# Performance work log

Measured on AMD Instinct MI355X. Metric: run time of the kernel, lower is better.

## Reference

```python
import jax, jax.numpy as jnp
import numpy as np
import math

B, L, DIM = 2, 2048, 1024
NUM_HEADS, QUANTUM_HEADS, CHUNK = 16, 2, 64
HD = DIM // NUM_HEADS  # 64 == CHUNK (required by the original broadcast)
TH = NUM_HEADS - QUANTUM_HEADS
STEPS = 2048
LN_EPS = 1e-5


def setup_inputs() -> dict:
    key = jax.random.key(0)
    ks = jax.random.split(key, 12)
    inp = {
        'x': jax.random.normal(ks[0], (B, L, DIM), dtype=jnp.float32),
        # to_quantum_state: Linear(HD, 2HD) + LayerNorm(2HD) + Tanh
        'wq1': jax.random.normal(ks[1], (HD, 2 * HD), dtype=jnp.float32) * 0.05,
        'bq1': jnp.zeros((2 * HD,), dtype=jnp.float32),
        'ln_g': jnp.ones((2 * HD,), dtype=jnp.float32),
        'ln_b': jnp.zeros((2 * HD,), dtype=jnp.float32),
        'phase_shifts': jax.random.normal(ks[2], (QUANTUM_HEADS,), dtype=jnp.float32) * 0.02,
        'freqs': jax.random.normal(ks[3], (QUANTUM_HEADS,), dtype=jnp.float32) * 0.02,
        # traditional heads: q/k/v projections, no bias
        'wq': jax.random.normal(ks[4], (DIM, TH * HD), dtype=jnp.float32) * 0.02,
        'wk': jax.random.normal(ks[5], (DIM, TH * HD), dtype=jnp.float32) * 0.02,
        'wv': jax.random.normal(ks[6], (DIM, TH * HD), dtype=jnp.float32) * 0.02,
        # output projection
        'wo': jax.random.normal(ks[7], (DIM, DIM), dtype=jnp.float32) * 0.02,
        'bo': jnp.zeros((DIM,), dtype=jnp.float32),
    }
    return inp


def _quantum_state(t, wq1, bq1, ln_g, ln_b):
    # Linear -> LayerNorm -> Tanh; split into (amp, phase)
    h = t @ wq1 + bq1
    mu = h.mean(-1, keepdims=True)
    var = ((h - mu) ** 2).mean(-1, keepdims=True)
    h = (h - mu) * jax.lax.rsqrt(var + LN_EPS) * ln_g + ln_b
    h = jnp.tanh(h)
    return h[..., :HD], h[..., HD:]


def reference(x, wq1, bq1, ln_g, ln_b, phase_shifts, freqs, wq, wk, wv, wo, bo):
    two_pi = 2.0 * math.pi
    angles = jnp.linspace(0.0, two_pi, STEPS)  # torch.linspace is endpoint-inclusive
    cos_table = jnp.cos(angles)
    inv_sqrt_hd = 1.0 / math.sqrt(HD)
    nc = L // CHUNK

    quantum_outs = []
    for h in range(QUANTUM_HEADS):
        xh = x[..., h * HD:(h + 1) * HD]                       # [B,L,HD]
        amp, phase = _quantum_state(xh, wq1, bq1, ln_g, ln_b)  # each [B,L,HD]
        qa = amp.reshape(B, nc, CHUNK, HD)
        qp = phase.reshape(B, nc, CHUNK, HD)
        # keys/values are truncated to the FIRST `chunk` tokens (original quirk)
        ka = amp[:, :CHUNK]        # [B,CHUNK,HD]
        kp = phase[:, :CHUNK]
        v = xh[:, :CHUNK]
        # phase_diff[b,c,i,j] = qp[b,c,i,j] - kp[b,j,i]  (needs CHUNK == HD)
        pd = (qp - jnp.swapaxes(kp, -1, -2)[:, None]) * freqs[h] + phase_shifts[h]
        idx = jnp.mod(pd / two_pi * STEPS, STEPS).astype(jnp.int32)  # in [0, STEPS)
        interference = cos_table[idx]                          # [B,nc,CHUNK,CHUNK]
        scores = jnp.einsum('bcih,bjh->bcij', qa, ka) * interference
        attn = jax.nn.softmax(scores * inv_sqrt_hd, axis=-1)
        out = jnp.einsum('bcij,bjh->bcih', attn, v).reshape(B, L, HD)
        quantum_outs.append(out)

    # traditional multi-head attention on full x
    q = (x @ wq).reshape(B, L, TH, HD)
    k = (x @ wk).reshape(B, L, TH, HD)
    vv = (x @ wv).reshape(B, L, TH, HD)
    scores = jnp.einsum('bqhd,bkhd->bhqk', q, k) * inv_sqrt_hd
    attn = jax.nn.softmax(scores, axis=-1)
    trad = jnp.einsum('bhqk,bkhd->bqhd', attn, vv).reshape(B, L, TH * HD)

    out = jnp.concatenate(quantum_outs + [trad], axis=-1)  # [B,L,DIM]
    return out @ wo + bo
```

## Files before the change

kernel.cpp:

```cpp
#include <hip/hip_runtime.h>
#include <hip/hip_bf16.h>
#include <math.h>

#define B_ 2
#define L_ 2048
#define DIM_ 1024
#define HD_ 64
#define TH_ 14
#define TWO_PI_F 6.28318530717958647692f
#define QSCALE_F 0.1803368801111204f

typedef __bf16 bf16_t;
typedef __bf16 bf16x8 __attribute__((ext_vector_type(8)));
typedef __bf16 bf16x4 __attribute__((ext_vector_type(4)));
typedef float f32x4 __attribute__((ext_vector_type(4)));
typedef float f32x16 __attribute__((ext_vector_type(16)));
typedef unsigned int u32x2 __attribute__((ext_vector_type(2)));

static __device__ __forceinline__ bf16_t f2b(float f) { return (bf16_t)f; }

static __device__ __forceinline__ float fexp2(float x) {
#if __has_builtin(__builtin_amdgcn_exp2f)
  return __builtin_amdgcn_exp2f(x);
#else
  return exp2f(x);
#endif
}

static __device__ __forceinline__ unsigned int cvtpk(float a, float b) {
  unsigned int r;
  asm("v_cvt_pk_bf16_f32 %0, %1, %2" : "=v"(r) : "v"(a), "v"(b));
  return r;
}

static __device__ __forceinline__ void gl16(const bf16_t* g, bf16_t* l) {
  __builtin_amdgcn_global_load_lds(
      (const __attribute__((address_space(1))) void*)g,
      (__attribute__((address_space(3))) void*)l, 16, 0, 0);
}

static __device__ __forceinline__ void swap32(unsigned int& a, unsigned int& b) {
#if __has_builtin(__builtin_amdgcn_permlane32_swap)
  u32x2 r = __builtin_amdgcn_permlane32_swap(a, b, false, false);
  a = r[0];
  b = r[1];
#else
  const int l = (int)(threadIdx.x & 63);
  unsigned int bp_a = (unsigned int)__builtin_amdgcn_ds_bpermute((l ^ 32) << 2, (int)a);
  unsigned int bp_b = (unsigned int)__builtin_amdgcn_ds_bpermute((l ^ 32) << 2, (int)b);
  unsigned int na = (l < 32) ? a : bp_b;
  unsigned int nb = (l < 32) ? bp_a : b;
  a = na;
  b = nb;
#endif
}

__global__ __launch_bounds__(256)
void k_prep(const float* __restrict__ x, const float* __restrict__ wq1,
            const float* __restrict__ bq1, const float* __restrict__ ln_g,
            const float* __restrict__ ln_b, const float* __restrict__ wq,
            const float* __restrict__ wk, const float* __restrict__ wv,
            const float* __restrict__ wo, bf16_t* __restrict__ xb,
            bf16_t* __restrict__ wt_qkv, bf16_t* __restrict__ wt_o,
            bf16_t* __restrict__ amp_b, float* __restrict__ phase) {
  __shared__ float tile[32][33];
  const int t = threadIdx.x;
  const int bid = blockIdx.x;
  if (bid < 4096) {
    const int i = bid * 256 + t;
    const float4 v4 = ((const float4*)x)[i];
    bf16x4 o = {f2b(v4.x), f2b(v4.y), f2b(v4.z), f2b(v4.w)};
    *(bf16x4*)(xb + 4 * (size_t)i) = o;
  } else if (bid < 7808) {
    const float* W;
    bf16_t* Wt;
    int N, kt, nt;
    if (bid < 6784) {
      int r = bid - 4096;
      const int which = r / 896;
      r -= which * 896;
      W = (which == 0) ? wq : (which == 1) ? wk : wv;
      Wt = wt_qkv + (size_t)which * 896 * 1024;
      N = 896;
      kt = r & 31;
      nt = r >> 5;
    } else {
      const int r = bid - 6784;
      W = wo;
      Wt = wt_o;
      N = 1024;
      kt = r & 31;
      nt = r >> 5;
    }
    const int tx = t & 31, ty = t >> 5;
    const int k0 = kt * 32, n0 = nt * 32;
    #pragma unroll
    for (int i = 0; i < 4; ++i)
      tile[ty + 8 * i][tx] = W[(size_t)(k0 + ty + 8 * i) * N + n0 + tx];
    __syncthreads();
    #pragma unroll
    for (int i = 0; i < 4; ++i)
      Wt[(size_t)(n0 + ty + 8 * i) * 1024 + k0 + tx] = f2b(tile[tx][ty + 8 * i]);
  } else {
    const int gw = ((bid - 7808) * 256 + t) >> 6;
    const int lane = t & 63;
    const int h = gw >> 12;
    const int bl = gw & 4095;
    const float xv = x[(size_t)bl * DIM_ + h * HD_ + lane];
    float acc0 = bq1[lane];
    float acc1 = bq1[64 + lane];
    #pragma unroll 16
    for (int kk = 0; kk < 64; ++kk) {
      const float xk = __shfl(xv, kk, 64);
      acc0 = fmaf(xk, wq1[kk * 128 + lane], acc0);
      acc1 = fmaf(xk, wq1[kk * 128 + 64 + lane], acc1);
    }
    float s = acc0 + acc1;
    #pragma unroll
    for (int off = 32; off > 0; off >>= 1) s += __shfl_xor(s, off, 64);
    const float mu = s * (1.0f / 128.0f);
    const float d0 = acc0 - mu, d1 = acc1 - mu;
    float vsum = d0 * d0 + d1 * d1;
    #pragma unroll
    for (int off = 32; off > 0; off >>= 1) vsum += __shfl_xor(vsum, off, 64);
    const float rstd = rsqrtf(vsum * (1.0f / 128.0f) + 1e-5f);
    const float av = tanhf(d0 * rstd * ln_g[lane] + ln_b[lane]);
    const float pv = tanhf(d1 * rstd * ln_g[64 + lane] + ln_b[64 + lane]);
    const size_t o = ((size_t)h * (B_ * L_) + bl) * HD_ + lane;
    amp_b[o] = f2b(av);
    phase[o] = pv;
  }
}

__global__ __launch_bounds__(256)
void k_mm1q(const bf16_t* __restrict__ A, const bf16_t* __restrict__ Wt,
            bf16_t* __restrict__ qb, bf16_t* __restrict__ kb, bf16_t* __restrict__ vb,
            const bf16_t* __restrict__ amp_b, const float* __restrict__ phase,
            const float* __restrict__ shifts, const float* __restrict__ freqs,
            bf16_t* __restrict__ catb) {
  __shared__ char smem[32768];
  const int t = threadIdx.x;
  const int lane = t & 63, w = t >> 6;
  const int bid = blockIdx.x;
  const int xcd = bid & 7, slot = bid >> 3;
  if (slot < 84) {
    bf16_t* Asm = (bf16_t*)smem;
    bf16_t* Bsm = (bf16_t*)(smem + 16384);
    const int wm = w >> 1, wn = w & 1;
    const int l31 = lane & 31, hi = lane >> 5;
    const int m_blk = xcd * 4 + slot / 21;
    const int n_blk = slot % 21;
    const int m0 = m_blk * 128;
    const int n0 = n_blk * 128;
    f32x16 acc[2][2] = {};
    for (int k0 = 0; k0 < 1024; k0 += 64) {
      __syncthreads();
      #pragma unroll
      for (int qc = 0; qc < 4; ++qc) {
        const int idx = t + 256 * qc;
        const int r = idx >> 3, cb = idx & 7;
        const int c = (cb ^ (r & 7)) * 8;
        gl16(A + (size_t)(m0 + r) * 1024 + k0 + c, Asm + w * 512 + qc * 2048);
        gl16(Wt + (size_t)(n0 + r) * 1024 + k0 + c, Bsm + w * 512 + qc * 2048);
      }
      __syncthreads();
      #pragma unroll
      for (int s = 0; s < 4; ++s) {
        const int ra0 = wm * 64 + l31, ra1 = ra0 + 32;
        const int rb0 = wn * 64 + l31, rb1 = rb0 + 32;
        const bf16x8 af0 = *(const bf16x8*)((char*)Asm + ra0 * 128 + (((2 * s + hi) ^ (ra0 & 7)) << 4));
        const bf16x8 af1 = *(const bf16x8*)((char*)Asm + ra1 * 128 + (((2 * s + hi) ^ (ra1 & 7)) << 4));
        const bf16x8 bf0 = *(const bf16x8*)((char*)Bsm + rb0 * 128 + (((2 * s + hi) ^ (rb0 & 7)) << 4));
        const bf16x8 bf1 = *(const bf16x8*)((char*)Bsm + rb1 * 128 + (((2 * s + hi) ^ (rb1 & 7)) << 4));
        acc[0][0] = __builtin_amdgcn_mfma_f32_32x32x16_bf16(bf0, af0, acc[0][0], 0, 0, 0);
        acc[0][1] = __builtin_amdgcn_mfma_f32_32x32x16_bf16(bf1, af0, acc[0][1], 0, 0, 0);
        acc[1][0] = __builtin_amdgcn_mfma_f32_32x32x16_bf16(bf0, af1, acc[1][0], 0, 0, 0);
        acc[1][1] = __builtin_amdgcn_mfma_f32_32x32x16_bf16(bf1, af1, acc[1][1], 0, 0, 0);
      }
    }
    const int n0w = n0 + wn * 64;
    const int which = (n0 >= 1792) ? 2 : (n0 >= 896) ? 1 : 0;
    #pragma unroll
    for (int mi = 0; mi < 2; ++mi) {
      const int m = m0 + wm * 64 + mi * 32 + l31;
      const int bsel = m >> 11, ll = m & 2047;
      #pragma unroll
      for (int ni = 0; ni < 2; ++ni) {
        if (which == 2) {
          #pragma unroll
          for (int rp = 0; rp < 4; ++rp) {
            #pragma unroll
            for (int e = 0; e < 4; ++e) {
              const int nn = n0w + ni * 32 + 8 * rp + 4 * hi + e - 1792;
              const int head = nn >> 6, hd = nn & 63;
              vb[(((size_t)bsel * TH_ + head) * HD_ + hd) * L_ + ll] = f2b(acc[mi][ni][4 * rp + e]);
            }
          }
        } else {
          const float sc = (which == 0) ? QSCALE_F : 1.0f;
          bf16_t* dst = (which == 0) ? qb : kb;
          #pragma unroll
          for (int rp = 0; rp < 4; ++rp) {
            const int nb = n0w + ni * 32 + 8 * rp + 4 * hi;
            const int nn = nb - which * 896;
            const int head = nn >> 6, hd = nn & 63;
            bf16x4 pk;
            #pragma unroll
            for (int e = 0; e < 4; ++e) pk[e] = f2b(acc[mi][ni][4 * rp + e] * sc);
            *(bf16x4*)(dst + (((size_t)bsel * TH_ + head) * L_ + ll) * HD_ + hd) = pk;
          }
        }
      }
    }
  } else {
    bf16_t* Kam = (bf16_t*)smem;
    bf16_t* Vt  = (bf16_t*)(smem + 8192);
    bf16_t* Ps  = (bf16_t*)(smem + 16384);
    const int l15 = lane & 15, g = lane >> 4;
    const int qv = xcd * 16 + (slot - 84);
    const int c = qv & 31;
    const int hb = qv >> 5;
    const int b = hb & 1;
    const int h = hb >> 1;
    const size_t abase = ((size_t)h * B_ + b) * L_ * HD_;

    {
      const int r0 = t >> 3, cb0 = t & 7;
      const int r1 = r0 + 32;
      gl16(amp_b + abase + r0 * 64 + (cb0 ^ (r0 & 7)) * 8, Kam + w * 512);
      gl16(amp_b + abase + r1 * 64 + (cb0 ^ (r1 & 7)) * 8, Kam + w * 512 + 2048);
    }
    {
      const int vj = t >> 2;
      const int vd0 = (t & 3) * 16;
      const bf16x8 va = *(const bf16x8*)(A + ((size_t)b * L_ + vj) * DIM_ + h * 64 + vd0);
      const bf16x8 vb2 = *(const bf16x8*)(A + ((size_t)b * L_ + vj) * DIM_ + h * 64 + vd0 + 8);
      #pragma unroll
      for (int e = 0; e < 8; ++e) {
        int d = vd0 + e;
        *(bf16_t*)((char*)Vt + d * 128 + (((vj >> 3) ^ (d & 7)) << 4) + (vj & 7) * 2) = va[e];
        d = vd0 + 8 + e;
        *(bf16_t*)((char*)Vt + d * 128 + (((vj >> 3) ^ (d & 7)) << 4) + (vj & 7) * 2) = vb2[e];
      }
    }
    __syncthreads();

    bf16x8 qf[2];
    {
      const size_t ro = abase + (size_t)(c * 64 + 16 * w + l15) * 64 + g * 8;
      qf[0] = *(const bf16x8*)(amp_b + ro);
      qf[1] = *(const bf16x8*)(amp_b + ro + 32);
    }
    f32x4 s[4] = {};
    #pragma unroll
    for (int ks = 0; ks < 2; ++ks) {
      #pragma unroll
      for (int nt = 0; nt < 4; ++nt) {
        const int jr = nt * 16 + l15;
        const bf16x8 kf = *(const bf16x8*)((char*)Kam + jr * 128 + (((ks * 4 + g) ^ (jr & 7)) << 4));
        s[nt] = __builtin_amdgcn_mfma_f32_16x16x32_bf16(qf[ks], kf, s[nt], 0, 0, 0);
      }
    }
    const float freq = freqs[h], shift = shifts[h];
    char* PsW = (char*)Ps + w * 2048;
    float l_acc[4];
    #pragma unroll
    for (int r = 0; r < 4; ++r) {
      const int i_loc = 16 * w + 4 * g + r;
      const float* qrow = phase + abase + (size_t)(c * 64 + i_loc) * 64;
      const float* krow = phase + abase + i_loc;
      const int row = g * 4 + r;
      float ls = 0.0f;
      #pragma unroll
      for (int nt = 0; nt < 4; ++nt) {
        const int j = nt * 16 + l15;
        const float qp = qrow[j];
        const float kp = krow[j * 64];
        const float pd = (qp - kp) * freq + shift;
        const float t1 = pd * (2048.0f / TWO_PI_F);
        float mm = fmodf(t1, 2048.0f);
        if (mm < 0.0f) mm += 2048.0f;
        int idx = (int)mm;
        idx = idx > 2047 ? 2047 : idx;
        const float interf = cosf((float)idx * (TWO_PI_F / 2047.0f));
        const float sc = s[nt][r] * interf * 0.125f;
        const float e = expf(sc);
        ls += e;
        *(bf16_t*)(PsW + row * 128 + (((j >> 3) ^ (row & 7)) << 4) + (j & 7) * 2) = f2b(e);
      }
      #pragma unroll
      for (int off = 1; off < 16; off <<= 1) ls += __shfl_xor(ls, off, 64);
      l_acc[r] = ls;
    }
    f32x4 o[4] = {};
    #pragma unroll
    for (int ks = 0; ks < 2; ++ks) {
      const bf16x8 pa = *(const bf16x8*)(PsW + l15 * 128 + (((ks * 4 + g) ^ (l15 & 7)) << 4));
      #pragma unroll
      for (int nt = 0; nt < 4; ++nt) {
        const int dr = nt * 16 + l15;
        const bf16x8 vf = *(const bf16x8*)((char*)Vt + dr * 128 + (((ks * 4 + g) ^ (dr & 7)) << 4));
        o[nt] = __builtin_amdgcn_mfma_f32_16x16x32_bf16(pa, vf, o[nt], 0, 0, 0);
      }
    }
    #pragma unroll
    for (int r = 0; r < 4; ++r) {
      const float inv = 1.0f / l_acc[r];
      const int qrow = c * 64 + 16 * w + g * 4 + r;
      #pragma unroll
      for (int nt = 0; nt < 4; ++nt)
        catb[((size_t)b * L_ + qrow) * DIM_ + h * 64 + nt * 16 + l15] = f2b(o[nt][r] * inv);
    }
  }
}

__global__ __launch_bounds__(256)
void k_mm0(const bf16_t* __restrict__ A, const bf16_t* __restrict__ Wt,
           const float* __restrict__ bias, float* __restrict__ outf) {
  __shared__ bf16_t Asm[128 * 64];
  __shared__ bf16_t Bsm[128 * 64];
  const int t = threadIdx.x;
  const int lane = t & 63, w = t >> 6;
  const int wm = w >> 1, wn = w & 1;
  const int l31 = lane & 31, hi = lane >> 5;
  const int bid = blockIdx.x;
  const int v = (bid & 7) * 32 + (bid >> 3);
  const int m0 = (v & 31) * 128;
  const int n0 = (v >> 5) * 128;
  f32x16 acc[2][2] = {};
  for (int k0 = 0; k0 < 1024; k0 += 64) {
    __syncthreads();
    #pragma unroll
    for (int qc = 0; qc < 4; ++qc) {
      const int idx = t + 256 * qc;
      const int r = idx >> 3, cb = idx & 7;
      const int c = (cb ^ (r & 7)) * 8;
      gl16(A + (size_t)(m0 + r) * 1024 + k0 + c, Asm + w * 512 + qc * 2048);
      gl16(Wt + (size_t)(n0 + r) * 1024 + k0 + c, Bsm + w * 512 + qc * 2048);
    }
    __syncthreads();
    #pragma unroll
    for (int s = 0; s < 4; ++s) {
      const int ra0 = wm * 64 + l31, ra1 = ra0 + 32;
      const int rb0 = wn * 64 + l31, rb1 = rb0 + 32;
      const bf16x8 af0 = *(const bf16x8*)((char*)Asm + ra0 * 128 + (((2 * s + hi) ^ (ra0 & 7)) << 4));
      const bf16x8 af1 = *(const bf16x8*)((char*)Asm + ra1 * 128 + (((2 * s + hi) ^ (ra1 & 7)) << 4));
      const bf16x8 bf0 = *(const bf16x8*)((char*)Bsm + rb0 * 128 + (((2 * s + hi) ^ (rb0 & 7)) << 4));
      const bf16x8 bf1 = *(const bf16x8*)((char*)Bsm + rb1 * 128 + (((2 * s + hi) ^ (rb1 & 7)) << 4));
      acc[0][0] = __builtin_amdgcn_mfma_f32_32x32x16_bf16(bf0, af0, acc[0][0], 0, 0, 0);
      acc[0][1] = __builtin_amdgcn_mfma_f32_32x32x16_bf16(bf1, af0, acc[0][1], 0, 0, 0);
      acc[1][0] = __builtin_amdgcn_mfma_f32_32x32x16_bf16(bf0, af1, acc[1][0], 0, 0, 0);
      acc[1][1] = __builtin_amdgcn_mfma_f32_32x32x16_bf16(bf1, af1, acc[1][1], 0, 0, 0);
    }
  }
  #pragma unroll
  for (int mi = 0; mi < 2; ++mi) {
    const int m = m0 + wm * 64 + mi * 32 + l31;
    #pragma unroll
    for (int ni = 0; ni < 2; ++ni) {
      #pragma unroll
      for (int rp = 0; rp < 4; ++rp) {
        const int nb = n0 + wn * 64 + ni * 32 + 8 * rp + 4 * hi;
        const float4 bv = *(const float4*)&bias[nb];
        float4 r4;
        r4.x = acc[mi][ni][4 * rp + 0] + bv.x;
        r4.y = acc[mi][ni][4 * rp + 1] + bv.y;
        r4.z = acc[mi][ni][4 * rp + 2] + bv.z;
        r4.w = acc[mi][ni][4 * rp + 3] + bv.w;
        *(float4*)&outf[(size_t)m * 1024 + nb] = r4;
      }
    }
  }
}

__global__ __launch_bounds__(512)
void k_flash2(const bf16_t* __restrict__ qg, const bf16_t* __restrict__ kg,
              const bf16_t* __restrict__ vt, bf16_t* __restrict__ catb) {
  __shared__ char smem[65536];
  const int t = threadIdx.x;
  const int lane = t & 63, w = t >> 6;
  const int g2 = w >> 2, wl = w & 3;
  const int l31 = lane & 31, hi = lane >> 5;
  int bid = blockIdx.x;
  bid = (bid & 7) * 56 + (bid >> 3);
  const int qblk = bid & 15, bh = bid >> 4;
  const int head = bh % TH_, b = bh / TH_;
  const size_t base = (size_t)bh * (L_ * HD_);
  const int q = qblk * 128 + wl * 32 + l31;
  const int tl = t & 255;
  const int r0 = tl >> 3, cb0 = tl & 7;
  const int r1 = r0 + 32;
  const int c0 = (cb0 ^ (r0 & 7)) * 8;
  const int c1 = (cb0 ^ (r1 & 7)) * 8;
  const int ubase = wl * 512;
  bf16_t* Kg = (bf16_t*)(smem + g2 * 32768);
  bf16_t* Vg = (bf16_t*)(smem + g2 * 32768 + 16384);
  const int kt0 = g2 * 16;

  bf16x8 qf[4];
  #pragma unroll
  for (int slot = 0; slot < 4; ++slot)
    qf[slot] = *(const bf16x8*)(qg + base + (size_t)q * 64 + 16 * slot + 8 * hi);

  f32x16 oT[2] = {};
  float l_acc = 0.0f;

  {
    const bf16_t* ksrc = kg + base + (size_t)kt0 * 64 * 64;
    const bf16_t* vsrc = vt + base + kt0 * 64;
    gl16(ksrc + r0 * 64 + c0, Kg + ubase);
    gl16(ksrc + r1 * 64 + c1, Kg + ubase + 2048);
    gl16(vsrc + (size_t)r0 * L_ + c0, Vg + ubase);
    gl16(vsrc + (size_t)r1 * L_ + c1, Vg + ubase + 2048);
  }
  for (int kt = 0; kt < 16; ++kt) {
    const int cur = kt & 1;
    if (kt < 15) {
      const bf16_t* ksrc = kg + base + (size_t)(kt0 + kt + 1) * 64 * 64;
      const bf16_t* vsrc = vt + base + (kt0 + kt + 1) * 64;
      bf16_t* kd = Kg + (cur ^ 1) * 4096;
      bf16_t* vd = Vg + (cur ^ 1) * 4096;
      gl16(ksrc + r0 * 64 + c0, kd + ubase);
      gl16(ksrc + r1 * 64 + c1, kd + ubase + 2048);
      gl16(vsrc + (size_t)r0 * L_ + c0, vd + ubase);
      gl16(vsrc + (size_t)r1 * L_ + c1, vd + ubase + 2048);
      asm volatile("s_waitcnt vmcnt(4)" ::: "memory");
    } else {
      asm volatile("s_waitcnt vmcnt(0)" ::: "memory");
    }
    __builtin_amdgcn_sched_barrier(0);
    __builtin_amdgcn_s_barrier();
    const char* Kc = (const char*)(Kg + cur * 4096);
    const char* Vc = (const char*)(Vg + cur * 4096);
    f32x16 sT0 = {}, sT1 = {};
    __builtin_amdgcn_s_setprio(1);
    #pragma unroll
    for (int slot = 0; slot < 4; ++slot) {
      const int row0 = l31;
      const int row1 = 32 + l31;
      const bf16x8 kf0 = *(const bf16x8*)(Kc + row0 * 128 + (((2 * slot + hi) ^ (row0 & 7)) << 4));
      const bf16x8 kf1 = *(const bf16x8*)(Kc + row1 * 128 + (((2 * slot + hi) ^ (row1 & 7)) << 4));
      sT0 = __builtin_amdgcn_mfma_f32_32x32x16_bf16(kf0, qf[slot], sT0, 0, 0, 0);
      sT1 = __builtin_amdgcn_mfma_f32_32x32x16_bf16(kf1, qf[slot], sT1, 0, 0, 0);
    }
    __builtin_amdgcn_s_setprio(0);
    unsigned int W0[8], W1[8];
    float la = 0.0f;
    #pragma unroll
    for (int rp = 0; rp < 8; ++rp) {
      const float p00 = fexp2(sT0[2 * rp]);
      const float p01 = fexp2(sT0[2 * rp + 1]);
      const float p10 = fexp2(sT1[2 * rp]);
      const float p11 = fexp2(sT1[2 * rp + 1]);
      la += (p00 + p01) + (p10 + p11);
      W0[rp] = cvtpk(p00, p01);
      W1[rp] = cvtpk(p10, p11);
    }
    l_acc += la;
    unsigned int pb[4][4];
    #pragma unroll
    for (int m1 = 0; m1 < 2; ++m1) {
      unsigned int u, vv;
      u = W0[m1];     vv = W0[2 + m1]; swap32(u, vv); pb[0][m1] = u; pb[0][m1 + 2] = vv;
      u = W0[4 + m1]; vv = W0[6 + m1]; swap32(u, vv); pb[1][m1] = u; pb[1][m1 + 2] = vv;
      u = W1[m1];     vv = W1[2 + m1]; swap32(u, vv); pb[2][m1] = u; pb[2][m1 + 2] = vv;
      u = W1[4 + m1]; vv = W1[6 + m1]; swap32(u, vv); pb[3][m1] = u; pb[3][m1 + 2] = vv;
    }
    __builtin_amdgcn_s_setprio(1);
    #pragma unroll
    for (int slot = 0; slot < 4; ++slot) {
      union { unsigned int u[4]; bf16x8 v8; } pf;
      pf.u[0] = pb[slot][0]; pf.u[1] = pb[slot][1];
      pf.u[2] = pb[slot][2]; pf.u[3] = pb[slot][3];
      #pragma unroll
      for (int dt = 0; dt < 2; ++dt) {
        const int row = 32 * dt + l31;
        const bf16x8 vf = *(const bf16x8*)(Vc + row * 128 + (((2 * slot + hi) ^ (row & 7)) << 4));
        oT[dt] = __builtin_amdgcn_mfma_f32_32x32x16_bf16(vf, pf.v8, oT[dt], 0, 0, 0);
      }
    }
    __builtin_amdgcn_s_setprio(0);
    __builtin_amdgcn_s_barrier();
  }
  const float l_w = l_acc + __shfl_xor(l_acc, 32, 64);
  __syncthreads();
  float* obuf = (float*)(smem + 32768);
  float* lbuf = (float*)smem;
  if (g2 == 1) {
    #pragma unroll
    for (int dt = 0; dt < 2; ++dt)
      #pragma unroll
      for (int e = 0; e < 16; ++e)
        obuf[(dt * 16 + e) * 256 + wl * 64 + lane] = oT[dt][e];
    lbuf[wl * 64 + lane] = l_w;
  }
  __syncthreads();
  if (g2 == 0) {
    const float l_tot = l_w + lbuf[wl * 64 + lane];
    const float inv = 1.0f / l_tot;
    const size_t obase = ((size_t)b * L_ + q) * DIM_ + 128 + head * 64;
    #pragma unroll
    for (int dt = 0; dt < 2; ++dt) {
      #pragma unroll
      for (int rq = 0; rq < 4; ++rq) {
        bf16x4 pk;
        #pragma unroll
        for (int e = 0; e < 4; ++e)
          pk[e] = f2b((oT[dt][4 * rq + e] +
                       obuf[(dt * 16 + 4 * rq + e) * 256 + wl * 64 + lane]) * inv);
        *(bf16x4*)(catb + obase + 32 * dt + 8 * rq + 4 * hi) = pk;
      }
    }
  }
}

extern "C" void kernel_launch(void* const* d_in, const int* in_sizes, int n_in,
                              void* d_out, int out_size, void* d_ws, size_t ws_size,
                              hipStream_t stream) {
  (void)in_sizes; (void)n_in; (void)out_size; (void)ws_size;
  const float* x      = (const float*)d_in[0];
  const float* wq1    = (const float*)d_in[1];
  const float* bq1    = (const float*)d_in[2];
  const float* ln_g   = (const float*)d_in[3];
  const float* ln_b   = (const float*)d_in[4];
  const float* shifts = (const float*)d_in[5];
  const float* freqs  = (const float*)d_in[6];
  const float* wq     = (const float*)d_in[7];
  const float* wk     = (const float*)d_in[8];
  const float* wv     = (const float*)d_in[9];
  const float* wo     = (const float*)d_in[10];
  const float* bo     = (const float*)d_in[11];
  float* out = (float*)d_out;

  char* p = (char*)d_ws;
  bf16_t* amp_b  = (bf16_t*)p; p += (size_t)2 * B_ * L_ * HD_ * 2;
  float* phase   = (float*)p;  p += (size_t)2 * B_ * L_ * HD_ * 4;
  bf16_t* xb     = (bf16_t*)p; p += (size_t)B_ * L_ * DIM_ * 2;
  bf16_t* wt_qkv = (bf16_t*)p; p += (size_t)2688 * 1024 * 2;
  bf16_t* wt_o   = (bf16_t*)p; p += (size_t)1024 * 1024 * 2;
  bf16_t* qb     = (bf16_t*)p; p += (size_t)B_ * TH_ * L_ * HD_ * 2;
  bf16_t* kb     = (bf16_t*)p; p += (size_t)B_ * TH_ * L_ * HD_ * 2;
  bf16_t* vtb    = (bf16_t*)p; p += (size_t)B_ * TH_ * L_ * HD_ * 2;
  bf16_t* catb   = (bf16_t*)p;

  k_prep<<<dim3(9856), dim3(256), 0, stream>>>(x, wq1, bq1, ln_g, ln_b,
                                               wq, wk, wv, wo,
                                               xb, wt_qkv, wt_o, amp_b, phase);
  k_mm1q<<<dim3(800), dim3(256), 0, stream>>>(xb, wt_qkv, qb, kb, vtb,
                                              amp_b, phase, shifts, freqs, catb);
  k_flash2<<<dim3(448), dim3(512), 0, stream>>>(qb, kb, vtb, catb);
  k_mm0<<<dim3(256), dim3(256), 0, stream>>>(catb, wt_o, bo, out);
}
```

Before: 121.0 us.

## Split flash attention key range across four wave groups with 32-key tiles

The flash-attention kernel now launches 1024 threads per block. Four wave groups each process a quarter of the key sequence in 32-key tiles, where before two groups each handled half in 64-key tiles. K/V shared-memory tiles shrink and V uses a narrower swizzle. Partial outputs and row sums are combined through a two-stage shared-memory tree reduction. The aim is more waves in flight for latency hiding, at the cost of extra reduction barriers and launch_bounds(1024, 8) register pressure.

```diff
diff --git a/kernel.cpp b/kernel.cpp
--- a/kernel.cpp
+++ b/kernel.cpp
@@ -373,7 +373,7 @@
   }
 }
 
-__global__ __launch_bounds__(512)
+__global__ __launch_bounds__(1024, 8)
 void k_flash2(const bf16_t* __restrict__ qg, const bf16_t* __restrict__ kg,
               const bf16_t* __restrict__ vt, bf16_t* __restrict__ catb) {
   __shared__ char smem[65536];
@@ -388,14 +388,13 @@
   const size_t base = (size_t)bh * (L_ * HD_);
   const int q = qblk * 128 + wl * 32 + l31;
   const int tl = t & 255;
-  const int r0 = tl >> 3, cb0 = tl & 7;
-  const int r1 = r0 + 32;
-  const int c0 = (cb0 ^ (r0 & 7)) * 8;
-  const int c1 = (cb0 ^ (r1 & 7)) * 8;
-  const int ubase = wl * 512;
-  bf16_t* Kg = (bf16_t*)(smem + g2 * 32768);
-  bf16_t* Vg = (bf16_t*)(smem + g2 * 32768 + 16384);
-  const int kt0 = g2 * 16;
+  const int kr = tl >> 3, kcb = tl & 7;
+  const int kc = (kcb ^ (kr & 7)) * 8;
+  const int vd = tl >> 2, vsl = tl & 3;
+  const int vc = (vsl ^ (vd & 3)) * 8;
+  bf16_t* Kg = (bf16_t*)(smem + g2 * 16384);
+  bf16_t* Vg = (bf16_t*)(smem + g2 * 16384 + 8192);
+  const int t0 = g2 * 16;
 
   bf16x8 qf[4];
   #pragma unroll
@@ -406,97 +405,100 @@
   float l_acc = 0.0f;
 
   {
-    const bf16_t* ksrc = kg + base + (size_t)kt0 * 64 * 64;
-    const bf16_t* vsrc = vt + base + kt0 * 64;
-    gl16(ksrc + r0 * 64 + c0, Kg + ubase);
-    gl16(ksrc + r1 * 64 + c1, Kg + ubase + 2048);
-    gl16(vsrc + (size_t)r0 * L_ + c0, Vg + ubase);
-    gl16(vsrc + (size_t)r1 * L_ + c1, Vg + ubase + 2048);
+    gl16(kg + base + (size_t)t0 * 2048 + kr * 64 + kc, Kg + tl * 8);
+    gl16(vt + base + (size_t)vd * L_ + t0 * 32 + vc, Vg + tl * 8);
   }
   for (int kt = 0; kt < 16; ++kt) {
     const int cur = kt & 1;
     if (kt < 15) {
-      const bf16_t* ksrc = kg + base + (size_t)(kt0 + kt + 1) * 64 * 64;
-      const bf16_t* vsrc = vt + base + (kt0 + kt + 1) * 64;
-      bf16_t* kd = Kg + (cur ^ 1) * 4096;
-      bf16_t* vd = Vg + (cur ^ 1) * 4096;
-      gl16(ksrc + r0 * 64 + c0, kd + ubase);
-      gl16(ksrc + r1 * 64 + c1, kd + ubase + 2048);
-      gl16(vsrc + (size_t)r0 * L_ + c0, vd + ubase);
-      gl16(vsrc + (size_t)r1 * L_ + c1, vd + ubase + 2048);
-      asm volatile("s_waitcnt vmcnt(4)" ::: "memory");
+      const int nt = t0 + kt + 1;
+      gl16(kg + base + (size_t)nt * 2048 + kr * 64 + kc, Kg + (cur ^ 1) * 2048 + tl * 8);
+      gl16(vt + base + (size_t)vd * L_ + nt * 32 + vc, Vg + (cur ^ 1) * 2048 + tl * 8);
+      asm volatile("s_waitcnt vmcnt(2)" ::: "memory");
     } else {
       asm volatile("s_waitcnt vmcnt(0)" ::: "memory");
     }
     __builtin_amdgcn_sched_barrier(0);
     __builtin_amdgcn_s_barrier();
-    const char* Kc = (const char*)(Kg + cur * 4096);
-    const char* Vc = (const char*)(Vg + cur * 4096);
-    f32x16 sT0 = {}, sT1 = {};
+    const char* Kc = (const char*)(Kg + cur * 2048);
+    const char* Vc = (const char*)(Vg + cur * 2048);
+    f32x16 sT = {};
     __builtin_amdgcn_s_setprio(1);
     #pragma unroll
     for (int slot = 0; slot < 4; ++slot) {
-      const int row0 = l31;
-      const int row1 = 32 + l31;
-      const bf16x8 kf0 = *(const bf16x8*)(Kc + row0 * 128 + (((2 * slot + hi) ^ (row0 & 7)) << 4));
-      const bf16x8 kf1 = *(const bf16x8*)(Kc + row1 * 128 + (((2 * slot + hi) ^ (row1 & 7)) << 4));
-      sT0 = __builtin_amdgcn_mfma_f32_32x32x16_bf16(kf0, qf[slot], sT0, 0, 0, 0);
-      sT1 = __builtin_amdgcn_mfma_f32_32x32x16_bf16(kf1, qf[slot], sT1, 0, 0, 0);
+      const bf16x8 kf = *(const bf16x8*)(Kc + l31 * 128 + (((2 * slot + hi) ^ (l31 & 7)) << 4));
+      sT = __builtin_amdgcn_mfma_f32_32x32x16_bf16(kf, qf[slot], sT, 0, 0, 0);
     }
     __builtin_amdgcn_s_setprio(0);
-    unsigned int W0[8], W1[8];
+    unsigned int W0[8];
     float la = 0.0f;
     #pragma unroll
     for (int rp = 0; rp < 8; ++rp) {
-      const float p00 = fexp2(sT0[2 * rp]);
-      const float p01 = fexp2(sT0[2 * rp + 1]);
-      const float p10 = fexp2(sT1[2 * rp]);
-      const float p11 = fexp2(sT1[2 * rp + 1]);
-      la += (p00 + p01) + (p10 + p11);
+      const float p00 = fexp2(sT[2 * rp]);
+      const float p01 = fexp2(sT[2 * rp + 1]);
+      la += p00 + p01;
       W0[rp] = cvtpk(p00, p01);
-      W1[rp] = cvtpk(p10, p11);
     }
     l_acc += la;
-    unsigned int pb[4][4];
+    unsigned int pb[2][4];
     #pragma unroll
     for (int m1 = 0; m1 < 2; ++m1) {
       unsigned int u, vv;
       u = W0[m1];     vv = W0[2 + m1]; swap32(u, vv); pb[0][m1] = u; pb[0][m1 + 2] = vv;
       u = W0[4 + m1]; vv = W0[6 + m1]; swap32(u, vv); pb[1][m1] = u; pb[1][m1 + 2] = vv;
-      u = W1[m1];     vv = W1[2 + m1]; swap32(u, vv); pb[2][m1] = u; pb[2][m1 + 2] = vv;
-      u = W1[4 + m1]; vv = W1[6 + m1]; swap32(u, vv); pb[3][m1] = u; pb[3][m1 + 2] = vv;
     }
     __builtin_amdgcn_s_setprio(1);
     #pragma unroll
-    for (int slot = 0; slot < 4; ++slot) {
+    for (int ks = 0; ks < 2; ++ks) {
       union { unsigned int u[4]; bf16x8 v8; } pf;
-      pf.u[0] = pb[slot][0]; pf.u[1] = pb[slot][1];
-      pf.u[2] = pb[slot][2]; pf.u[3] = pb[slot][3];
+      pf.u[0] = pb[ks][0]; pf.u[1] = pb[ks][1];
+      pf.u[2] = pb[ks][2]; pf.u[3] = pb[ks][3];
       #pragma unroll
       for (int dt = 0; dt < 2; ++dt) {
-        const int row = 32 * dt + l31;
-        const bf16x8 vf = *(const bf16x8*)(Vc + row * 128 + (((2 * slot + hi) ^ (row & 7)) << 4));
+        const int dr = 32 * dt + l31;
+        const bf16x8 vf = *(const bf16x8*)(Vc + dr * 64 + (((2 * ks + hi) ^ (dr & 3)) << 4));
         oT[dt] = __builtin_amdgcn_mfma_f32_32x32x16_bf16(vf, pf.v8, oT[dt], 0, 0, 0);
       }
     }
     __builtin_amdgcn_s_setprio(0);
     __builtin_amdgcn_s_barrier();
   }
-  const float l_w = l_acc + __shfl_xor(l_acc, 32, 64);
+  float l2 = l_acc + __shfl_xor(l_acc, 32, 64);
   __syncthreads();
-  float* obuf = (float*)(smem + 32768);
-  float* lbuf = (float*)smem;
+  float* fb = (float*)smem;
+  const int tid = wl * 64 + lane;
+  if (g2 >= 2) {
+    #pragma unroll
+    for (int j = 0; j < 16; ++j) fb[(g2 - 2) * 4096 + j * 256 + tid] = oT[0][j];
+    fb[8192 + (g2 - 2) * 256 + tid] = l2;
+  }
+  __syncthreads();
+  if (g2 < 2) {
+    #pragma unroll
+    for (int j = 0; j < 16; ++j) oT[0][j] += fb[g2 * 4096 + j * 256 + tid];
+    l2 += fb[8192 + g2 * 256 + tid];
+  }
+  __syncthreads();
+  if (g2 >= 2) {
+    #pragma unroll
+    for (int j = 0; j < 16; ++j) fb[(g2 - 2) * 4096 + j * 256 + tid] = oT[1][j];
+  }
+  __syncthreads();
+  if (g2 < 2) {
+    #pragma unroll
+    for (int j = 0; j < 16; ++j) oT[1][j] += fb[g2 * 4096 + j * 256 + tid];
+  }
+  __syncthreads();
   if (g2 == 1) {
     #pragma unroll
     for (int dt = 0; dt < 2; ++dt)
       #pragma unroll
-      for (int e = 0; e < 16; ++e)
-        obuf[(dt * 16 + e) * 256 + wl * 64 + lane] = oT[dt][e];
-    lbuf[wl * 64 + lane] = l_w;
+      for (int j = 0; j < 16; ++j) fb[(dt * 16 + j) * 256 + tid] = oT[dt][j];
+    fb[8192 + tid] = l2;
   }
   __syncthreads();
   if (g2 == 0) {
-    const float l_tot = l_w + lbuf[wl * 64 + lane];
+    const float l_tot = l2 + fb[8192 + tid];
     const float inv = 1.0f / l_tot;
     const size_t obase = ((size_t)b * L_ + q) * DIM_ + 128 + head * 64;
     #pragma unroll
@@ -507,7 +509,7 @@
         #pragma unroll
         for (int e = 0; e < 4; ++e)
           pk[e] = f2b((oT[dt][4 * rq + e] +
-                       obuf[(dt * 16 + 4 * rq + e) * 256 + wl * 64 + lane]) * inv);
+                       fb[(dt * 16 + 4 * rq + e) * 256 + tid]) * inv);
         *(bf16x4*)(catb + obase + 32 * dt + 8 * rq + 4 * hi) = pk;
       }
     }
@@ -548,6 +550,6 @@
                                                xb, wt_qkv, wt_o, amp_b, phase);
   k_mm1q<<<dim3(800), dim3(256), 0, stream>>>(xb, wt_qkv, qb, kb, vtb,
                                               amp_b, phase, shifts, freqs, catb);
-  k_flash2<<<dim3(448), dim3(512), 0, stream>>>(qb, kb, vtb, catb);
+  k_flash2<<<dim3(448), dim3(1024), 0, stream>>>(qb, kb, vtb, catb);
   k_mm0<<<dim3(256), dim3(256), 0, stream>>>(catb, wt_o, bo, out);
 }
```

New measurement: 195.3 us. 1.61x slower.
